# Optimization experiments

Measured on AMD Instinct MI355X. Metric: run time of the kernel, lower is better.

## Reference

```python
import jax, jax.numpy as jnp
import numpy as np

LN_EPS = 1e-5
NORM_EPS = 1e-12  # F.normalize eps


def _l2norm(x):
    # torch F.normalize(p=2, dim=-1): x / max(||x||, eps)
    n = jnp.sqrt(jnp.sum(x * x, axis=-1, keepdims=True))
    return x / jnp.maximum(n, NORM_EPS)


def setup_inputs() -> dict:
    key = jax.random.key(0)
    D, R, H = 256, 32, 64  # d_model, rank, d_model//4
    B, C, P = 32, 64, 96
    ks = jax.random.split(key, 16)
    s = 0.05
    return {
        "x": jax.random.normal(ks[0], (B * C, P, D), jnp.float32),
        "ln_gamma": jnp.ones((D,), jnp.float32),
        "ln_beta": jnp.zeros((D,), jnp.float32),
        "Wd": jax.random.normal(ks[1], (D, R), jnp.float32) * s,
        "bd": jax.random.normal(ks[2], (R,), jnp.float32) * s,
        "Wq": jax.random.normal(ks[3], (R, R), jnp.float32) * s,
        "Wk": jax.random.normal(ks[4], (R, R), jnp.float32) * s,
        "Wv": jax.random.normal(ks[5], (R, R), jnp.float32) * s,
        "Wg": jax.random.normal(ks[6], (R, R), jnp.float32) * s,
        "bg": jax.random.normal(ks[7], (R,), jnp.float32) * s,
        "Wu": jax.random.normal(ks[8], (R, D), jnp.float32) * s,
        "bu": jax.random.normal(ks[9], (D,), jnp.float32) * s,
        "W1": jax.random.normal(ks[10], (D, H), jnp.float32) * s,
        "b1": jax.random.normal(ks[11], (H,), jnp.float32) * s,
        "W2": jax.random.normal(ks[12], (H, D), jnp.float32) * s,
        "b2": jnp.full((D,), -5.0, jnp.float32),  # gate_init bias
        "B": B,
        "C": C,
    }


def reference(x, ln_gamma, ln_beta, Wd, bd, Wq, Wk, Wv, Wg, bg, Wu, bu, W1, b1, W2, b2, B, C):
    BC, P, D = x.shape
    # [B*C, P, D] -> [B*P, C, D] channel-mixing layout
    h = x.reshape(B, C, P, D).transpose(0, 2, 1, 3).reshape(B * P, C, D)

    # LayerNorm over D (biased variance, as in torch LayerNorm)
    mu = jnp.mean(h, axis=-1, keepdims=True)
    var = jnp.var(h, axis=-1, keepdims=True)
    h_norm = (h - mu) * jax.lax.rsqrt(var + LN_EPS) * ln_gamma + ln_beta

    # bottleneck projection to rank R
    h_low = h_norm @ Wd + bd  # [BP, C, R]

    # Hydra linear attention: cosine-normalized Q/K, sum-pooled K*V global feature
    Q = _l2norm(h_low @ Wq)
    K = _l2norm(h_low @ Wk)
    V = h_low @ Wv
    global_feat = jnp.sum(K * V, axis=1, keepdims=True)  # [BP, 1, R]
    h_attn = Q * global_feat

    # content gate and up-projection
    gate_c = jax.nn.sigmoid(h_low @ Wg + bg)
    mixed = (h_attn * gate_c) @ Wu + bu  # [BP, C, D]

    # AdaptiveGate: unbiased variance over channel dim (torch .var default ddof=1)
    chan_var = jnp.var(h, axis=1, ddof=1)  # [BP, D]
    gate_logits = jax.nn.gelu(chan_var @ W1 + b1, approximate=False) @ W2 + b2
    gate = jax.nn.sigmoid(gate_logits)[:, None, :]  # [BP, 1, D]

    out = h + gate * mixed
    # back to [B*C, P, D]
    return out.reshape(B, P, C, D).transpose(0, 2, 1, 3).reshape(BC, P, D)
```

## Files before the change

### kernel.cpp

```cpp
#include <hip/hip_runtime.h>
#include <hip/hip_bf16.h>

#define DD 256
#define RR 32
#define CC 64
#define PB 96
#define NT 1024

typedef __attribute__((ext_vector_type(8))) short short8;
typedef __attribute__((ext_vector_type(4))) float f32x4;

__device__ __forceinline__ short f2bf(float f) {
    return __builtin_bit_cast(short, __float2bfloat16(f));
}
__device__ __forceinline__ float b2f(unsigned short s) {
    union { unsigned u; float f; } v; v.u = ((unsigned)s) << 16;
    return v.f;
}

__device__ __forceinline__ int hswz(int c, int d) {
    return c * 256 + (d ^ ((c & 7) << 3));
}
__device__ __forceinline__ int nswz(int r, int k) {
    return r * 32 + (k ^ (((r >> 1) & 3) << 3));
}

__global__ __launch_bounds__(1024, 1)
void prep_kernel(const float* __restrict__ ln_g, const float* __restrict__ ln_b,
                 const float* __restrict__ Wd, const float* __restrict__ bd,
                 const float* __restrict__ Wq, const float* __restrict__ Wk,
                 const float* __restrict__ Wv, const float* __restrict__ Wg,
                 const float* __restrict__ Wu,
                 const float* __restrict__ W1, const float* __restrict__ W2,
                 short* __restrict__ wsWd, short* __restrict__ wsQKVG,
                 short* __restrict__ wsF3, float* __restrict__ wsLN,
                 float* __restrict__ wsW1T, float* __restrict__ wsW2T)
{
    __shared__ float redp[2048];
    const int t = threadIdx.x;
    {
        const int r = t >> 5, dblk = t & 31;
        short8 vv;
        float sa = 0.f, sb = 0.f;
        #pragma unroll
        for (int j = 0; j < 8; ++j) {
            const int d = dblk * 8 + j;
            const float wd = Wd[d * RR + r];
            const float g  = ln_g[d];
            vv[j] = f2bf(g * wd);
            sa += g * wd;
            sb += ln_b[d] * wd;
        }
        *(short8*)&wsWd[r * 256 + ((dblk ^ (r & 7)) << 3)] = vv;
        redp[r * 32 + dblk]        = sa;
        redp[1024 + r * 32 + dblk] = sb;
    }
    if (t < 512) {
        const int m = t >> 7, rr2 = (t >> 2) & 31, kg = t & 3;
        const float* Wm = (m == 0) ? Wq : (m == 1) ? Wk : (m == 2) ? Wv : Wg;
        short8 vv;
        #pragma unroll
        for (int j = 0; j < 8; ++j)
            vv[j] = f2bf(Wm[(kg * 8 + j) * RR + rr2]);
        *(short8*)&wsQKVG[m * 1024 + rr2 * 32 + ((kg ^ ((rr2 >> 1) & 3)) << 3)] = vv;
    }
    {
        const int f = t >> 6, l = t & 63;
        const int d = f * 16 + (l & 15);
        short8 v;
        #pragma unroll
        for (int j = 0; j < 8; ++j) {
            const int r = (l >> 4) * 8 + j;
            v[j] = f2bf(Wu[r * DD + d]);
        }
        *(short8*)&wsF3[f * 512 + l * 8] = v;
    }
    #pragma unroll
    for (int rep = 0; rep < 16; ++rep) {
        const int id = rep * 1024 + t;
        const int j = id >> 8, d = id & 255;
        wsW1T[j * 256 + d] = W1[d * 64 + j];
    }
    #pragma unroll
    for (int rep = 0; rep < 16; ++rep) {
        const int id = rep * 1024 + t;
        const int d = id >> 6, j = id & 63;
        wsW2T[d * 64 + j] = W2[j * 256 + d];
    }
    __syncthreads();
    if (t < 32) {
        float s = 0.f;
        #pragma unroll
        for (int g = 0; g < 32; ++g) s += redp[t * 32 + g];
        wsLN[t] = s;
    } else if (t < 64) {
        const int r = t - 32;
        float s = 0.f;
        #pragma unroll
        for (int g = 0; g < 32; ++g) s += redp[1024 + r * 32 + g];
        wsLN[t] = s + bd[r];
    }
}

__global__ __launch_bounds__(NT, 8)
void hydra_kernel(const float* __restrict__ x,
                  const short* __restrict__ wsWd, const short* __restrict__ wsQKVG,
                  const short* __restrict__ wsF3, const float* __restrict__ wsLN,
                  const float* __restrict__ wsW1T, const float* __restrict__ wsW2T,
                  const float* __restrict__ bg,
                  const float* __restrict__ bu,
                  const float* __restrict__ b1, const float* __restrict__ b2,
                  float* __restrict__ out)
{
    __shared__ short hbf[CC * DD];
    __shared__ short wreg[RR * DD];
    __shared__ short qg[CC * RR];
    __shared__ short lowbuf[CC * RR];
    __shared__ float redB[2048];
    __shared__ float redC[1024];
    __shared__ float gfp[128];
    __shared__ float mu_s[CC], rstd_s[CC];
    __shared__ float cv_s[DD], gate_s[DD];
    __shared__ float hid_s[64];
    __shared__ float ln_a[RR], ln_bv[RR];

    const int t    = threadIdx.x;
    const int lane = t & 63;
    const int w    = t >> 6;
    const int bp   = blockIdx.x;
    const int b    = bp / PB;
    const int p    = bp - b * PB;
    const size_t rowbase = (size_t)(b * CC) * PB * DD + (size_t)p * DD;

    #pragma unroll
    for (int i = 0; i < 4; ++i) {
        const int c = w * 4 + i;
        const float4 v = *(const float4*)(x + rowbase + (size_t)c * (PB * DD) + 4 * lane);
        float s1 = v.x + v.y + v.z + v.w;
        float s2 = v.x * v.x + v.y * v.y + v.z * v.z + v.w * v.w;
        s1 += __shfl_xor(s1, 1, 64); s2 += __shfl_xor(s2, 1, 64);
        s1 += __shfl_xor(s1, 2, 64); s2 += __shfl_xor(s2, 2, 64);
        s1 += __shfl_xor(s1, 4, 64); s2 += __shfl_xor(s2, 4, 64);
        if ((lane & 7) == 0)
            *(float2*)&redC[(c * 8 + (lane >> 3)) * 2] = make_float2(s1, s2);
        ushort4 pk;
        pk.x = (unsigned short)f2bf(v.x); pk.y = (unsigned short)f2bf(v.y);
        pk.z = (unsigned short)f2bf(v.z); pk.w = (unsigned short)f2bf(v.w);
        *(ushort4*)&hbf[hswz(c, 4 * lane)] = pk;
    }
    *(short8*)&wreg[t * 8] = *(const short8*)&wsWd[t * 8];
    if (t < 32)              ln_a[t]       = wsLN[t];
    else if (t < 64)         ln_bv[t - 32] = wsLN[t];
    __syncthreads();

    f32x4 s3acc = {0.f, 0.f, 0.f, 0.f};
    if (w < 8) {
        const int ct = w >> 1, rt = w & 1;
        const int arow = ct * 16 + (lane & 15);
        const int brow = rt * 16 + (lane & 15);
        const int ksub = lane >> 4;
        #pragma unroll
        for (int step = 0; step < 8; ++step) {
            const short8 a  = *(const short8*)&hbf[hswz(arow, step * 32 + ksub * 8)];
            const short8 bf = *(const short8*)&wreg[hswz(brow, step * 32 + ksub * 8)];
            s3acc = __builtin_amdgcn_mfma_f32_16x16x32_bf16(a, bf, s3acc, 0, 0, 0);
        }
    } else {
        const int idx = t - 512;
        const int dp  = idx & 127;
        const int rg  = idx >> 7;
        const int d0  = dp * 2;
        float s1a = 0.f, s1b = 0.f, s2a = 0.f, s2b = 0.f;
        #pragma unroll
        for (int i = 0; i < 16; ++i) {
            const int c = rg * 16 + i;
            const ushort2 u = *(const ushort2*)&hbf[hswz(c, d0)];
            const float va = b2f(u.x), vb = b2f(u.y);
            s1a += va; s2a += va * va;
            s1b += vb; s2b += vb * vb;
        }
        *(float2*)&redB[rg * 256 + d0]        = make_float2(s1a, s1b);
        *(float2*)&redB[1024 + rg * 256 + d0] = make_float2(s2a, s2b);
        if (idx < 64) {
            const int c = idx;
            float s1 = 0.f, s2 = 0.f;
            #pragma unroll
            for (int g = 0; g < 8; ++g) {
                const float2 pr = *(const float2*)&redC[(c * 8 + g) * 2];
                s1 += pr.x; s2 += pr.y;
            }
            const float mu = s1 * (1.f / 256.f);
            mu_s[c]   = mu;
            rstd_s[c] = rsqrtf(s2 * (1.f / 256.f) - mu * mu + 1e-5f);
        }
    }
    __syncthreads();

    if (w < 8) {
        const int ct = w >> 1, rt = w & 1;
        const int col = rt * 16 + (lane & 15);
        const float la = ln_a[col], lb = ln_bv[col];
        #pragma unroll
        for (int i = 0; i < 4; ++i) {
            const int c = ct * 16 + (lane >> 4) * 4 + i;
            const float rs = rstd_s[c];
            const float hl = rs * s3acc[i] - rs * mu_s[c] * la + lb;
            lowbuf[nswz(c, col)] = f2bf(hl);
        }
    } else {
        const int idx = t - 512;
        *(short8*)&wreg[idx * 8] = *(const short8*)&wsQKVG[idx * 8];
    }
    if (t < 256) {
        const float S1 = redB[t] + redB[256 + t] + redB[512 + t] + redB[768 + t];
        const float S2 = redB[1024 + t] + redB[1280 + t] + redB[1536 + t] + redB[1792 + t];
        cv_s[t] = (S2 - S1 * S1 * (1.f / 64.f)) * (1.f / 63.f);
    }
    __syncthreads();

    if (w < 8) {
        const int ct = w >> 1, pair = w & 1;
        const int mA = pair ? 1 : 0;
        const int mB = pair ? 2 : 3;
        const int arow = ct * 16 + (lane & 15);
        const int ksub = lane >> 4;
        const short8 a = *(const short8*)&lowbuf[nswz(arow, ksub * 8)];
        f32x4 aA0 = {0,0,0,0}, aA1 = {0,0,0,0}, aB0 = {0,0,0,0}, aB1 = {0,0,0,0};
        {
            const int br0 = (lane & 15), br1 = 16 + (lane & 15);
            const short8 bA0 = *(const short8*)&wreg[mA * 1024 + nswz(br0, ksub * 8)];
            const short8 bA1 = *(const short8*)&wreg[mA * 1024 + nswz(br1, ksub * 8)];
            const short8 bB0 = *(const short8*)&wreg[mB * 1024 + nswz(br0, ksub * 8)];
            const short8 bB1 = *(const short8*)&wreg[mB * 1024 + nswz(br1, ksub * 8)];
            aA0 = __builtin_amdgcn_mfma_f32_16x16x32_bf16(a, bA0, aA0, 0, 0, 0);
            aA1 = __builtin_amdgcn_mfma_f32_16x16x32_bf16(a, bA1, aA1, 0, 0, 0);
            aB0 = __builtin_amdgcn_mfma_f32_16x16x32_bf16(a, bB0, aB0, 0, 0, 0);
            aB1 = __builtin_amdgcn_mfma_f32_16x16x32_bf16(a, bB1, aB1, 0, 0, 0);
        }
        float qs[4];
        #pragma unroll
        for (int i = 0; i < 4; ++i) {
            float ss = aA0[i] * aA0[i] + aA1[i] * aA1[i];
            ss += __shfl_xor(ss, 1, 64);
            ss += __shfl_xor(ss, 2, 64);
            ss += __shfl_xor(ss, 4, 64);
            ss += __shfl_xor(ss, 8, 64);
            qs[i] = 1.f / fmaxf(sqrtf(ss), 1e-12f);
        }
        const int col0 = (lane & 15), col1 = 16 + (lane & 15);
        if (pair == 0) {
            const float bgv0 = bg[col0], bgv1 = bg[col1];
            #pragma unroll
            for (int i = 0; i < 4; ++i) {
                const int c = ct * 16 + (lane >> 4) * 4 + i;
                const float g0 = 1.f / (1.f + __expf(-(aB0[i] + bgv0)));
                const float g1 = 1.f / (1.f + __expf(-(aB1[i] + bgv1)));
                qg[c * 32 + col0] = f2bf(aA0[i] * qs[i] * g0);
                qg[c * 32 + col1] = f2bf(aA1[i] * qs[i] * g1);
            }
        } else {
            float p0 = 0.f, p1 = 0.f;
            #pragma unroll
            for (int i = 0; i < 4; ++i) {
                p0 += (aA0[i] * qs[i]) * aB0[i];
                p1 += (aA1[i] * qs[i]) * aB1[i];
            }
            p0 += __shfl_xor(p0, 16, 64); p1 += __shfl_xor(p1, 16, 64);
            p0 += __shfl_xor(p0, 32, 64); p1 += __shfl_xor(p1, 32, 64);
            if (lane < 16) {
                gfp[ct * 32 + lane]      = p0;
                gfp[ct * 32 + 16 + lane] = p1;
            }
        }
    } else {
        const int j = (w - 8) * 8 + (lane >> 3);
        const int q = lane & 7;
        const float* w1row = wsW1T + j * 256 + q * 32;
        float s = 0.f;
        #pragma unroll
        for (int ii = 0; ii < 8; ++ii) {
            const float4 wv  = *(const float4*)(w1row + ii * 4);
            const float4 cvv = *(const float4*)&cv_s[q * 32 + ii * 4];
            s += cvv.x * wv.x + cvv.y * wv.y + cvv.z * wv.z + cvv.w * wv.w;
        }
        s += __shfl_xor(s, 1, 64);
        s += __shfl_xor(s, 2, 64);
        s += __shfl_xor(s, 4, 64);
        if (q == 0) {
            const float z = s + b1[j];
            hid_s[j] = 0.5f * z * (1.f + erff(z * 0.70710678118654752f));
        }
    }
    __syncthreads();

    if (t < 256) {
        const int r = t & 31, c0 = t >> 5, c1 = (t >> 5) + 32;
        const float gf = gfp[r] + gfp[32 + r] + gfp[64 + r] + gfp[96 + r];
        lowbuf[nswz(c0, r)] = f2bf(b2f((unsigned short)qg[c0 * 32 + r]) * gf);
        lowbuf[nswz(c1, r)] = f2bf(b2f((unsigned short)qg[c1 * 32 + r]) * gf);
    } else if (t < 512) {
        const int d = t - 256;
        const float* w2row = wsW2T + d * 64;
        float s = b2[d];
        #pragma unroll
        for (int ii = 0; ii < 16; ++ii) {
            const float4 wv = *(const float4*)(w2row + ii * 4);
            const float4 hv = *(const float4*)&hid_s[ii * 4];
            s += hv.x * wv.x + hv.y * wv.y + hv.z * wv.z + hv.w * wv.w;
        }
        gate_s[d] = 1.f / (1.f + __expf(-s));
    }
    __syncthreads();

    {
        const int ct = w & 3, dg = w >> 2;
        const int arow = ct * 16 + (lane & 15);
        const int ksub = lane >> 4;
        const short8 a = *(const short8*)&lowbuf[nswz(arow, ksub * 8)];
        #pragma unroll
        for (int j = 0; j < 4; ++j) {
            const int dt = dg * 4 + j;
            const int col = dt * 16 + (lane & 15);
            const short8 bf = *(const short8*)(wsF3 + dt * 512 + lane * 8);
            f32x4 acc = {0.f, 0.f, 0.f, 0.f};
            acc = __builtin_amdgcn_mfma_f32_16x16x32_bf16(a, bf, acc, 0, 0, 0);
            const float gt  = gate_s[col];
            const float buv = bu[col];
            #pragma unroll
            for (int i = 0; i < 4; ++i) {
                const int c = ct * 16 + (lane >> 4) * 4 + i;
                const float xv = b2f((unsigned short)hbf[hswz(c, col)]);
                out[rowbase + (size_t)c * (PB * DD) + col] = xv + gt * (acc[i] + buv);
            }
        }
    }
}

extern "C" void kernel_launch(void* const* d_in, const int* in_sizes, int n_in,
                              void* d_out, int out_size, void* d_ws, size_t ws_size,
                              hipStream_t stream) {
    (void)in_sizes; (void)n_in; (void)out_size; (void)ws_size;
    const float* x    = (const float*)d_in[0];
    const float* ln_g = (const float*)d_in[1];
    const float* ln_b = (const float*)d_in[2];
    const float* Wd   = (const float*)d_in[3];
    const float* bd   = (const float*)d_in[4];
    const float* Wq   = (const float*)d_in[5];
    const float* Wk   = (const float*)d_in[6];
    const float* Wv   = (const float*)d_in[7];
    const float* Wg   = (const float*)d_in[8];
    const float* bg   = (const float*)d_in[9];
    const float* Wu   = (const float*)d_in[10];
    const float* bu   = (const float*)d_in[11];
    const float* W1   = (const float*)d_in[12];
    const float* b1   = (const float*)d_in[13];
    const float* W2   = (const float*)d_in[14];
    const float* b2   = (const float*)d_in[15];
    float* out = (float*)d_out;

    short* wsWd   = (short*)d_ws;
    short* wsQKVG = wsWd + 8192;
    short* wsF3   = wsQKVG + 4096;
    float* wsLN   = (float*)(wsWd + 20480);
    float* wsW1T  = wsLN + 64;
    float* wsW2T  = wsW1T + 16384;

    prep_kernel<<<dim3(1), dim3(1024), 0, stream>>>(
        ln_g, ln_b, Wd, bd, Wq, Wk, Wv, Wg, Wu, W1, W2,
        wsWd, wsQKVG, wsF3, wsLN, wsW1T, wsW2T);
    hydra_kernel<<<dim3(32 * PB), dim3(NT), 0, stream>>>(
        x, wsWd, wsQKVG, wsF3, wsLN, wsW1T, wsW2T, bg, bu, b1, b2, out);
}
```

Before: 159.6 us.

## Restructure stage schedule to drop a barrier and fuse global-feature scaling

The channel-variance reduction is now done per column by 256 threads, with no split across row groups, so the redB scratch buffer and its second-stage reduction are removed. The W1 GELU hidden computation moves one stage earlier, and the Q*gate*global_feat scaling is folded into the up-projection operand load. That fold removes one __syncthreads and one intermediate LDS pass. In exchange, each of those 256 threads does a longer serial loop over 64 channels, and every wave redundantly sums the gfp partials.

After: 159.2 us. No clear change (-0.3%).

```diff
diff --git a/kernel.cpp b/kernel.cpp
--- a/kernel.cpp
+++ b/kernel.cpp
@@ -116,7 +116,6 @@
     __shared__ short wreg[RR * DD];
     __shared__ short qg[CC * RR];
     __shared__ short lowbuf[CC * RR];
-    __shared__ float redB[2048];
     __shared__ float redC[1024];
     __shared__ float gfp[128];
     __shared__ float mu_s[CC], rstd_s[CC];
@@ -165,34 +164,26 @@
             const short8 bf = *(const short8*)&wreg[hswz(brow, step * 32 + ksub * 8)];
             s3acc = __builtin_amdgcn_mfma_f32_16x16x32_bf16(a, bf, s3acc, 0, 0, 0);
         }
-    } else {
-        const int idx = t - 512;
-        const int dp  = idx & 127;
-        const int rg  = idx >> 7;
-        const int d0  = dp * 2;
-        float s1a = 0.f, s1b = 0.f, s2a = 0.f, s2b = 0.f;
-        #pragma unroll
-        for (int i = 0; i < 16; ++i) {
-            const int c = rg * 16 + i;
-            const ushort2 u = *(const ushort2*)&hbf[hswz(c, d0)];
-            const float va = b2f(u.x), vb = b2f(u.y);
-            s1a += va; s2a += va * va;
-            s1b += vb; s2b += vb * vb;
-        }
-        *(float2*)&redB[rg * 256 + d0]        = make_float2(s1a, s1b);
-        *(float2*)&redB[1024 + rg * 256 + d0] = make_float2(s2a, s2b);
-        if (idx < 64) {
-            const int c = idx;
-            float s1 = 0.f, s2 = 0.f;
-            #pragma unroll
-            for (int g = 0; g < 8; ++g) {
-                const float2 pr = *(const float2*)&redC[(c * 8 + g) * 2];
-                s1 += pr.x; s2 += pr.y;
-            }
-            const float mu = s1 * (1.f / 256.f);
-            mu_s[c]   = mu;
-            rstd_s[c] = rsqrtf(s2 * (1.f / 256.f) - mu * mu + 1e-5f);
-        }
+    } else if (t < 768) {
+        const int d = t - 512;
+        float s1 = 0.f, s2 = 0.f;
+        #pragma unroll 8
+        for (int c = 0; c < CC; ++c) {
+            const float v = b2f((unsigned short)hbf[hswz(c, d)]);
+            s1 += v; s2 += v * v;
+        }
+        cv_s[d] = (s2 - s1 * s1 * (1.f / 64.f)) * (1.f / 63.f);
+    } else if (t < 832) {
+        const int c = t - 768;
+        float s1 = 0.f, s2 = 0.f;
+        #pragma unroll
+        for (int g = 0; g < 8; ++g) {
+            const float2 pr = *(const float2*)&redC[(c * 8 + g) * 2];
+            s1 += pr.x; s2 += pr.y;
+        }
+        const float mu = s1 * (1.f / 256.f);
+        mu_s[c]   = mu;
+        rstd_s[c] = rsqrtf(s2 * (1.f / 256.f) - mu * mu + 1e-5f);
     }
     __syncthreads();
 
@@ -207,14 +198,25 @@
             const float hl = rs * s3acc[i] - rs * mu_s[c] * la + lb;
             lowbuf[nswz(c, col)] = f2bf(hl);
         }
+        *(short8*)&wreg[t * 8] = *(const short8*)&wsQKVG[t * 8];
     } else {
-        const int idx = t - 512;
-        *(short8*)&wreg[idx * 8] = *(const short8*)&wsQKVG[idx * 8];
-    }
-    if (t < 256) {
-        const float S1 = redB[t] + redB[256 + t] + redB[512 + t] + redB[768 + t];
-        const float S2 = redB[1024 + t] + redB[1280 + t] + redB[1536 + t] + redB[1792 + t];
-        cv_s[t] = (S2 - S1 * S1 * (1.f / 64.f)) * (1.f / 63.f);
+        const int j = (w - 8) * 8 + (lane >> 3);
+        const int q = lane & 7;
+        const float* w1row = wsW1T + j * 256 + q * 32;
+        float s = 0.f;
+        #pragma unroll
+        for (int ii = 0; ii < 8; ++ii) {
+            const float4 wv  = *(const float4*)(w1row + ii * 4);
+            const float4 cvv = *(const float4*)&cv_s[q * 32 + ii * 4];
+            s += cvv.x * wv.x + cvv.y * wv.y + cvv.z * wv.z + cvv.w * wv.w;
+        }
+        s += __shfl_xor(s, 1, 64);
+        s += __shfl_xor(s, 2, 64);
+        s += __shfl_xor(s, 4, 64);
+        if (q == 0) {
+            const float z = s + b1[j];
+            hid_s[j] = 0.5f * z * (1.f + erff(z * 0.70710678118654752f));
+        }
     }
     __syncthreads();
 
@@ -255,8 +257,8 @@
                 const int c = ct * 16 + (lane >> 4) * 4 + i;
                 const float g0 = 1.f / (1.f + __expf(-(aB0[i] + bgv0)));
                 const float g1 = 1.f / (1.f + __expf(-(aB1[i] + bgv1)));
-                qg[c * 32 + col0] = f2bf(aA0[i] * qs[i] * g0);
-                qg[c * 32 + col1] = f2bf(aA1[i] * qs[i] * g1);
+                qg[nswz(c, col0)] = f2bf(aA0[i] * qs[i] * g0);
+                qg[nswz(c, col1)] = f2bf(aA1[i] * qs[i] * g1);
             }
         } else {
             float p0 = 0.f, p1 = 0.f;
@@ -272,34 +274,8 @@
                 gfp[ct * 32 + 16 + lane] = p1;
             }
         }
-    } else {
-        const int j = (w - 8) * 8 + (lane >> 3);
-        const int q = lane & 7;
-        const float* w1row = wsW1T + j * 256 + q * 32;
-        float s = 0.f;
-        #pragma unroll
-        for (int ii = 0; ii < 8; ++ii) {
-            const float4 wv  = *(const float4*)(w1row + ii * 4);
-            const float4 cvv = *(const float4*)&cv_s[q * 32 + ii * 4];
-            s += cvv.x * wv.x + cvv.y * wv.y + cvv.z * wv.z + cvv.w * wv.w;
-        }
-        s += __shfl_xor(s, 1, 64);
-        s += __shfl_xor(s, 2, 64);
-        s += __shfl_xor(s, 4, 64);
-        if (q == 0) {
-            const float z = s + b1[j];
-            hid_s[j] = 0.5f * z * (1.f + erff(z * 0.70710678118654752f));
-        }
-    }
-    __syncthreads();
-
-    if (t < 256) {
-        const int r = t & 31, c0 = t >> 5, c1 = (t >> 5) + 32;
-        const float gf = gfp[r] + gfp[32 + r] + gfp[64 + r] + gfp[96 + r];
-        lowbuf[nswz(c0, r)] = f2bf(b2f((unsigned short)qg[c0 * 32 + r]) * gf);
-        lowbuf[nswz(c1, r)] = f2bf(b2f((unsigned short)qg[c1 * 32 + r]) * gf);
-    } else if (t < 512) {
-        const int d = t - 256;
+    } else if (t < 768) {
+        const int d = t - 512;
         const float* w2row = wsW2T + d * 64;
         float s = b2[d];
         #pragma unroll
@@ -315,8 +291,31 @@
     {
         const int ct = w & 3, dg = w >> 2;
         const int arow = ct * 16 + (lane & 15);
-        const int ksub = lane >> 4;
-        const short8 a = *(const short8*)&lowbuf[nswz(arow, ksub * 8)];
+        const int kofs = (lane >> 4) * 8;
+        float gfv[8];
+        {
+            const float4 a0 = *(const float4*)&gfp[0 * 32 + kofs];
+            const float4 b0 = *(const float4*)&gfp[0 * 32 + kofs + 4];
+            const float4 a1 = *(const float4*)&gfp[1 * 32 + kofs];
+            const float4 b1v = *(const float4*)&gfp[1 * 32 + kofs + 4];
+            const float4 a2 = *(const float4*)&gfp[2 * 32 + kofs];
+            const float4 b2v = *(const float4*)&gfp[2 * 32 + kofs + 4];
+            const float4 a3 = *(const float4*)&gfp[3 * 32 + kofs];
+            const float4 b3 = *(const float4*)&gfp[3 * 32 + kofs + 4];
+            gfv[0] = a0.x + a1.x + a2.x + a3.x;
+            gfv[1] = a0.y + a1.y + a2.y + a3.y;
+            gfv[2] = a0.z + a1.z + a2.z + a3.z;
+            gfv[3] = a0.w + a1.w + a2.w + a3.w;
+            gfv[4] = b0.x + b1v.x + b2v.x + b3.x;
+            gfv[5] = b0.y + b1v.y + b2v.y + b3.y;
+            gfv[6] = b0.z + b1v.z + b2v.z + b3.z;
+            gfv[7] = b0.w + b1v.w + b2v.w + b3.w;
+        }
+        const short8 qv = *(const short8*)&qg[nswz(arow, kofs)];
+        short8 a;
+        #pragma unroll
+        for (int j = 0; j < 8; ++j)
+            a[j] = f2bf(b2f((unsigned short)qv[j]) * gfv[j]);
         #pragma unroll
         for (int j = 0; j < 4; ++j) {
             const int dt = dg * 4 + j;
```
